# Performance work log

Hardware: AMD Instinct MI355X
Metric: run time of the kernel (lower is better)

## Reference

```python
import jax, jax.numpy as jnp
import numpy as np

# ---------- static mesh topology helpers (numpy, setup-time only) ----------

def _topo_subdivide(nv, faces):
    edge_id = {}
    mids = []
    nf = []
    def mid(a, b):
        k = (a, b) if a < b else (b, a)
        if k not in edge_id:
            edge_id[k] = nv + len(mids)
            mids.append(k)
        return edge_id[k]
    for a, b, c in faces:
        a, b, c = int(a), int(b), int(c)
        ab, bc, ca = mid(a, b), mid(b, c), mid(c, a)
        nf += [[a, ab, ca], [b, bc, ab], [c, ca, bc], [ab, bc, ca]]
    return np.array(nf, dtype=np.int64), np.array(mids, dtype=np.int64)

def _icosphere(level, radius):
    t = (1.0 + 5.0 ** 0.5) / 2.0
    v = np.array([[-1, t, 0], [1, t, 0], [-1, -t, 0], [1, -t, 0],
                  [0, -1, t], [0, 1, t], [0, -1, -t], [0, 1, -t],
                  [t, 0, -1], [t, 0, 1], [-t, 0, -1], [-t, 0, 1]], dtype=np.float64)
    v /= np.linalg.norm(v, axis=1, keepdims=True)
    f = np.array([[0, 11, 5], [0, 5, 1], [0, 1, 7], [0, 7, 10], [0, 10, 11],
                  [1, 5, 9], [5, 11, 4], [11, 10, 2], [10, 7, 6], [7, 1, 8],
                  [3, 9, 4], [3, 4, 2], [3, 2, 6], [3, 6, 8], [3, 8, 9],
                  [4, 9, 5], [2, 4, 11], [6, 2, 10], [8, 6, 7], [9, 8, 1]], dtype=np.int64)
    for _ in range(level):
        f, mids = _topo_subdivide(len(v), f)
        mv = v[mids[:, 0]] + v[mids[:, 1]]
        mv /= np.linalg.norm(mv, axis=1, keepdims=True)
        v = np.concatenate([v, mv], 0)
    return (v * radius).astype(np.float32), f

def _directed_edges(faces):
    e = np.concatenate([faces[:, [0, 1]], faces[:, [1, 2]], faces[:, [2, 0]],
                        faces[:, [1, 0]], faces[:, [2, 1]], faces[:, [0, 2]]], 0)
    return np.unique(e, axis=0).T.astype(np.int64)  # (2, E) directed, deduped

# ---------- jax forward math ----------

def _project(verts, camera_c, camera_f):
    # K @ [I | t], t = (0,0,0.8): rows [f0,0,c0,0.8*c0],[0,f1,c1,0.8*c1],[0,0,1,0.8]
    z = jnp.zeros((), verts.dtype); o = jnp.ones((), verts.dtype)
    tz = jnp.asarray(0.8, verts.dtype)
    P = jnp.stack([
        jnp.stack([camera_f[0], z, camera_c[0], tz * camera_c[0]]),
        jnp.stack([z, camera_f[1], camera_c[1], tz * camera_c[1]]),
        jnp.stack([z, z, o, tz])])
    hom = jnp.concatenate([verts, jnp.ones((verts.shape[0], 1), verts.dtype)], 1)
    pc = hom @ P.T                     # (V, 3)
    return pc[:, :2] / pc[:, 2:3]      # (V, 2) pixel coords [x, y]

def _bilerp(feat, px, py, image_size):
    # feat: (C, dim, dim); px, py: (V,)
    dim = feat.shape[1]
    x = px * dim / image_size
    y = py * dim / image_size
    x1 = jnp.floor(x); x2 = x1 + 1.0
    y1 = jnp.floor(y); y2 = y1 + 1.0
    xi1 = jnp.clip(x1.astype(jnp.int32), 0, dim - 1)
    xi2 = jnp.clip(x2.astype(jnp.int32), 0, dim - 1)
    yi1 = jnp.clip(y1.astype(jnp.int32), 0, dim - 1)
    yi2 = jnp.clip(y2.astype(jnp.int32), 0, dim - 1)
    f11 = feat[:, xi1, yi1].T  # (V, C)
    f12 = feat[:, xi1, yi2].T
    f21 = feat[:, xi2, yi1].T
    f22 = feat[:, xi2, yi2].T
    w11 = ((x2 - x) * (y2 - y))[:, None]
    w12 = ((x2 - x) * (y - y1))[:, None]
    w21 = ((x - x1) * (y2 - y))[:, None]
    w22 = ((x - x1) * (y - y1))[:, None]
    return w11 * f11 + w12 * f12 + w21 * f21 + w22 * f22

def _gconv(x, W0, W1, b, src, dst):
    agg = jax.ops.segment_sum(x[dst], src, num_segments=x.shape[0])
    return x @ W0 + agg @ W1 + b

def _gresnet(x, edges, params):
    Win0, Win1, bin_, W0s, W1s, bs, Wc0, Wc1, bc = params
    src, dst = edges[0], edges[1]
    h = jax.nn.relu(_gconv(x, Win0, Win1, bin_, src, dst))
    def body(h, lw):
        W0, W1, b = lw
        return jax.nn.relu(_gconv(h, W0, W1, b, src, dst)) + h, None
    h, _ = jax.lax.scan(body, h, (W0s, W1s, bs))
    coords = _gconv(h, Wc0, Wc1, bc, src, dst)
    return h, coords

def _forward(f3, f4, f5, verts0, camera_c, camera_f, p1, p2, p3,
             edges1, edges2, edges3, mid0, mid1, image_size):
    def deform(verts, shape_feat, edges, params):
        pix = _project(verts, camera_c, camera_f)
        px, py = pix[:, 0], pix[:, 1]
        perc = jnp.concatenate([_bilerp(f3, px, py, image_size),
                                _bilerp(f4, px, py, image_size),
                                _bilerp(f5, px, py, image_size)], 1)  # (V, 1280)
        feats = jnp.concatenate([perc, shape_feat], 1)
        h, coords = _gresnet(feats, edges, params)
        return coords, h
    def unpool(verts, feat, mid):
        vf = jnp.concatenate([verts, feat], 1)
        new = (vf[mid[:, 0]] + vf[mid[:, 1]]) * 0.5  # edge midpoints
        vf = jnp.concatenate([vf, new], 0)
        return vf[:, :3], vf[:, 3:]
    verts, feat = deform(verts0, verts0, edges1, p1)
    verts, feat = unpool(verts, feat, mid0)
    verts, feat = deform(verts, feat, edges2, p2)
    verts, feat = unpool(verts, feat, mid1)
    verts, _ = deform(verts, feat, edges3, p3)
    return verts  # (40962, 3)

# ---------- harness entry points ----------

def setup_inputs() -> dict:
    key = jax.random.key(0)
    keys = iter(jax.random.split(key, 64))
    v0, f0 = _icosphere(4, 0.2)                      # 2562 verts, 5120 faces
    f1, mid0 = _topo_subdivide(len(v0), f0)          # -> 10242 verts topology
    f2, mid1 = _topo_subdivide(len(v0) + len(mid0), f1)  # -> 40962 verts
    inp = {
        'f3': jax.random.normal(next(keys), (256, 56, 56), jnp.float32),
        'f4': jax.random.normal(next(keys), (512, 28, 28), jnp.float32),
        'f5': jax.random.normal(next(keys), (512, 14, 14), jnp.float32),
        'verts0': jnp.asarray(v0),
        'camera_c': jnp.array([112.0, 112.0], jnp.float32),
        'camera_f': jnp.array([248.0, 248.0], jnp.float32),
    }
    D, L = 128, 12
    def stage(prefix, in_dim):
        def w(shape, scale):
            return jax.random.normal(next(keys), shape, jnp.float32) * scale
        inp[prefix + '_Win0'] = w((in_dim, D), 1.0 / np.sqrt(in_dim))
        inp[prefix + '_Win1'] = w((in_dim, D), 1.0 / np.sqrt(in_dim))
        inp[prefix + '_bin'] = jnp.zeros((D,), jnp.float32)
        inp[prefix + '_W0'] = w((L, D, D), 0.3 / np.sqrt(D))
        inp[prefix + '_W1'] = w((L, D, D), 0.3 / np.sqrt(D))
        inp[prefix + '_b'] = jnp.zeros((L, D), jnp.float32)
        inp[prefix + '_Wc0'] = w((D, 3), 0.01 / np.sqrt(D))
        inp[prefix + '_Wc1'] = w((D, 3), 0.01 / np.sqrt(D))
        inp[prefix + '_bc'] = jnp.zeros((3,), jnp.float32)
    stage('g1', 1283)
    stage('g2', 1408)
    stage('g3', 1408)
    inp['edges1'] = jnp.asarray(_directed_edges(f0))   # (2, 15360)
    inp['edges2'] = jnp.asarray(_directed_edges(f1))   # (2, 61440)
    inp['edges3'] = jnp.asarray(_directed_edges(f2))   # (2, 245760)
    inp['mid0'] = jnp.asarray(mid0)                    # (7680, 2)
    inp['mid1'] = jnp.asarray(mid1)                    # (30720, 2)
    inp['image_size'] = 224
    return inp

def reference(f3, f4, f5, verts0, camera_c, camera_f,
              g1_Win0, g1_Win1, g1_bin, g1_W0, g1_W1, g1_b, g1_Wc0, g1_Wc1, g1_bc,
              g2_Win0, g2_Win1, g2_bin, g2_W0, g2_W1, g2_b, g2_Wc0, g2_Wc1, g2_bc,
              g3_Win0, g3_Win1, g3_bin, g3_W0, g3_W1, g3_b, g3_Wc0, g3_Wc1, g3_bc,
              edges1, edges2, edges3, mid0, mid1, image_size):
    p1 = (g1_Win0, g1_Win1, g1_bin, g1_W0, g1_W1, g1_b, g1_Wc0, g1_Wc1, g1_bc)
    p2 = (g2_Win0, g2_Win1, g2_bin, g2_W0, g2_W1, g2_b, g2_Wc0, g2_Wc1, g2_bc)
    p3 = (g3_Win0, g3_Win1, g3_bin, g3_W0, g3_W1, g3_b, g3_Wc0, g3_Wc1, g3_bc)
    return _forward(f3, f4, f5, verts0, camera_c, camera_f, p1, p2, p3,
                    edges1, edges2, edges3, mid0, mid1, image_size)
```

## Files before the change

kernel.cpp:

```cpp
#include <hip/hip_runtime.h>
#include <hip/hip_bf16.h>
#include <cstddef>
#include <cstdint>

#define DIV_UP(a, b) (((a) + (b) - 1) / (b))

typedef __attribute__((ext_vector_type(8))) short bf16x8v;
typedef __attribute__((ext_vector_type(4))) float f32x4v;

__device__ __forceinline__ unsigned short bf16_rn(float v) {
    unsigned int u = __float_as_uint(v);
    unsigned int r = (u + 0x7FFFu + ((u >> 16) & 1u)) >> 16;
    return (unsigned short)r;
}
__device__ __forceinline__ float bf16_f(unsigned short h) {
    return __uint_as_float(((unsigned int)h) << 16);
}
__device__ __forceinline__ void f2hl(float v, unsigned short& hi, unsigned short& lo) {
    hi = bf16_rn(v);
    float r = v - bf16_f(hi);
    lo = bf16_rn(r);
}

__global__ void transpose_hl(const float* __restrict__ in, unsigned short* __restrict__ ohi,
                             unsigned short* __restrict__ olo, int C, int HW) {
    int idx = blockIdx.x * 256 + threadIdx.x;
    if (idx >= C * HW) return;
    int c = idx % C;
    int p = idx / C;
    float v = in[(size_t)c * HW + p];
    unsigned short hi, lo;
    f2hl(v, hi, lo);
    ohi[(size_t)p * C + c] = hi;
    olo[(size_t)p * C + c] = lo;
}

__global__ void pack_gb_bt(const float* __restrict__ W00, const float* __restrict__ W01,
                           const float* __restrict__ W10, const float* __restrict__ W11,
                           const float* __restrict__ W20, const float* __restrict__ W21,
                           unsigned short* __restrict__ Bhi, unsigned short* __restrict__ Blo,
                           int base, int C) {
    int idx = blockIdx.x * 256 + threadIdx.x;
    if (idx >= 768 * C) return;
    int n = idx / C, k = idx % C;
    int s = n >> 8, j = n & 255;
    const float* W0 = (s == 0) ? W00 : (s == 1) ? W10 : W20;
    const float* W1 = (s == 0) ? W01 : (s == 1) ? W11 : W21;
    float v = (j < 128) ? W0[(size_t)(base + k) * 128 + j]
                        : W1[(size_t)(base + k) * 128 + (j - 128)];
    unsigned short hi, lo;
    f2hl(v, hi, lo);
    Bhi[idx] = hi;
    Blo[idx] = lo;
}

__global__ void pack_lay_bt(const float* __restrict__ W0, const float* __restrict__ W1,
                            unsigned short* __restrict__ Bhi, unsigned short* __restrict__ Blo) {
    int idx = blockIdx.x * 256 + threadIdx.x;
    int l = idx >> 15;
    int r = idx & 32767;
    int n = r >> 8, k = r & 255;
    float v = (k < 128) ? W0[(size_t)l * 16384 + k * 128 + n]
                        : W1[(size_t)l * 16384 + (k - 128) * 128 + n];
    unsigned short hi, lo;
    f2hl(v, hi, lo);
    Bhi[idx] = hi;
    Blo[idx] = lo;
}

__global__ void pack_sh_bt(const float* __restrict__ Win0, const float* __restrict__ Win1,
                           unsigned short* __restrict__ Bhi, unsigned short* __restrict__ Blo) {
    int idx = blockIdx.x * 256 + threadIdx.x;
    if (idx >= 256 * 128) return;
    int n = idx >> 7, k = idx & 127;
    float v = (n < 128) ? Win0[(size_t)(1280 + k) * 128 + n]
                        : Win1[(size_t)(1280 + k) * 128 + (n - 128)];
    unsigned short hi, lo;
    f2hl(v, hi, lo);
    Bhi[idx] = hi;
    Blo[idx] = lo;
}

__global__ void desc_kernel(const float* __restrict__ verts,
                            const float* __restrict__ cam_c, const float* __restrict__ cam_f,
                            const int* __restrict__ imgsz, int V,
                            int* __restrict__ sampi, float* __restrict__ sampw) {
    int v = blockIdx.x * 256 + threadIdx.x;
    if (v >= V) return;
    float X = verts[3 * v + 0], Yy = verts[3 * v + 1], Z = verts[3 * v + 2];
    float cx = cam_c[0], cy = cam_c[1], fx = cam_f[0], fy = cam_f[1];
    const float tz = 0.8f;
    float pz = Z + tz;
    float px = (fx * X + cx * Z + tz * cx) / pz;
    float py = (fy * Yy + cy * Z + tz * cy) / pz;
    float is = (float)imgsz[0];
    const int Ss[3] = {56, 28, 14};
#pragma unroll
    for (int m = 0; m < 3; ++m) {
        int S = Ss[m];
        float dim = (float)S;
        float x = px * dim / is;
        float y = py * dim / is;
        float x1 = floorf(x), y1 = floorf(y);
        float x2 = x1 + 1.0f, y2 = y1 + 1.0f;
        float smax = (float)(S - 1);
        int xi1 = (int)fminf(fmaxf(x1, 0.0f), smax);
        int xi2 = (int)fminf(fmaxf(x2, 0.0f), smax);
        int yi1 = (int)fminf(fmaxf(y1, 0.0f), smax);
        int yi2 = (int)fminf(fmaxf(y2, 0.0f), smax);
        int b = v * 12 + m * 4;
        sampi[b + 0] = xi1 * S + yi1;
        sampi[b + 1] = xi1 * S + yi2;
        sampi[b + 2] = xi2 * S + yi1;
        sampi[b + 3] = xi2 * S + yi2;
        sampw[b + 0] = (x2 - x) * (y2 - y);
        sampw[b + 1] = (x2 - x) * (y - y1);
        sampw[b + 2] = (x - x1) * (y2 - y);
        sampw[b + 3] = (x - x1) * (y - y1);
    }
}

__global__ void rowptr_kernel(const int* __restrict__ src, int E, int V, int* __restrict__ rowptr) {
    int v = blockIdx.x * 256 + threadIdx.x;
    if (v > V) return;
    int lo = 0, hi = E;
    while (lo < hi) {
        int mid = (lo + hi) >> 1;
        if (src[mid] < v) lo = mid + 1; else hi = mid;
    }
    rowptr[v] = lo;
}

struct MArgs {
    const unsigned short *Ahi, *Alo; int lda;
    const unsigned short *Bhi, *Blo; int K;
    float* Y;
    int sstr;
    int V;
};

template <int EPI>
__global__ __launch_bounds__(256) void mgemm(MArgs g) {
    __shared__ unsigned short As_hi[64][40], As_lo[64][40];
    __shared__ unsigned short Bs_hi[128][40], Bs_lo[128][40];
    int tid = threadIdx.x;
    int row0 = blockIdx.y * 64;
    int col0 = blockIdx.x * 128;
    int l = tid & 63, wid = tid >> 6;
    int wr = wid & 1, wc = wid >> 1;
    int lw = l & 15, gg = l >> 4;
    f32x4v acc[2][4];
#pragma unroll
    for (int i = 0; i < 2; ++i)
#pragma unroll
        for (int j = 0; j < 4; ++j) acc[i][j] = (f32x4v){0.f, 0.f, 0.f, 0.f};

    int arow = tid >> 2, akoff = (tid & 3) * 8;
    for (int k0 = 0; k0 < g.K; k0 += 32) {
        __syncthreads();
        {
            int grow = row0 + arow;
            uint4 zh = make_uint4(0, 0, 0, 0), zl = make_uint4(0, 0, 0, 0);
            if (grow < g.V) {
                zh = *(const uint4*)(g.Ahi + (size_t)grow * g.lda + k0 + akoff);
                zl = *(const uint4*)(g.Alo + (size_t)grow * g.lda + k0 + akoff);
            }
            *(uint4*)&As_hi[arow][akoff] = zh;
            *(uint4*)&As_lo[arow][akoff] = zl;
        }
#pragma unroll
        for (int it = 0; it < 2; ++it) {
            int q = tid + it * 256;
            int n = q >> 2, koff = (q & 3) * 8;
            *(uint4*)&Bs_hi[n][koff] = *(const uint4*)(g.Bhi + (size_t)(col0 + n) * g.K + k0 + koff);
            *(uint4*)&Bs_lo[n][koff] = *(const uint4*)(g.Blo + (size_t)(col0 + n) * g.K + k0 + koff);
        }
        __syncthreads();
        bf16x8v ah[2], al[2], bh[4], bl[4];
#pragma unroll
        for (int mt = 0; mt < 2; ++mt) {
            int r = wr * 32 + mt * 16 + lw;
            ah[mt] = *(const bf16x8v*)&As_hi[r][gg * 8];
            al[mt] = *(const bf16x8v*)&As_lo[r][gg * 8];
        }
#pragma unroll
        for (int nt = 0; nt < 4; ++nt) {
            int c = wc * 64 + nt * 16 + lw;
            bh[nt] = *(const bf16x8v*)&Bs_hi[c][gg * 8];
            bl[nt] = *(const bf16x8v*)&Bs_lo[c][gg * 8];
        }
#pragma unroll
        for (int mt = 0; mt < 2; ++mt)
#pragma unroll
            for (int nt = 0; nt < 4; ++nt) {
                acc[mt][nt] = __builtin_amdgcn_mfma_f32_16x16x32_bf16(ah[mt], bh[nt], acc[mt][nt], 0, 0, 0);
                acc[mt][nt] = __builtin_amdgcn_mfma_f32_16x16x32_bf16(ah[mt], bl[nt], acc[mt][nt], 0, 0, 0);
                acc[mt][nt] = __builtin_amdgcn_mfma_f32_16x16x32_bf16(al[mt], bh[nt], acc[mt][nt], 0, 0, 0);
            }
    }
#pragma unroll
    for (int mt = 0; mt < 2; ++mt)
#pragma unroll
        for (int nt = 0; nt < 4; ++nt) {
            int colg = wc * 64 + nt * 16 + lw;
#pragma unroll
            for (int r = 0; r < 4; ++r) {
                int rowg = row0 + wr * 32 + mt * 16 + gg * 4 + r;
                if (rowg >= g.V) continue;
                float v = acc[mt][nt][r];
                if (EPI == 0) {
                    g.Y[(size_t)rowg * 256 + col0 + colg] += v;
                } else {
                    int cg = col0 + colg;
                    g.Y[(size_t)(cg >> 8) * g.sstr + (size_t)rowg * 256 + (cg & 255)] = v;
                }
            }
        }
}

__global__ void gather_kernel(const float* __restrict__ G, int sstr,
                              const int* __restrict__ sampi, const float* __restrict__ sampw,
                              float* __restrict__ Yb, int V, int stage,
                              const float* __restrict__ Win0, const float* __restrict__ Win1,
                              const float* __restrict__ shape) {
    int v = blockIdx.x;
    if (v >= V) return;
    int j = threadIdx.x;
    const float* Gs = G + (size_t)stage * sstr;
    int b = v * 12;
    float acc = 0.0f;
#pragma unroll
    for (int s = 0; s < 4; ++s)
        acc += sampw[b + s] * Gs[(size_t)sampi[b + s] * 256 + j];
#pragma unroll
    for (int s = 0; s < 4; ++s)
        acc += sampw[b + 4 + s] * Gs[(size_t)(3136 + sampi[b + 4 + s]) * 256 + j];
#pragma unroll
    for (int s = 0; s < 4; ++s)
        acc += sampw[b + 8 + s] * Gs[(size_t)(3920 + sampi[b + 8 + s]) * 256 + j];
    if (stage == 0) {
#pragma unroll
        for (int k = 0; k < 3; ++k) {
            float w = shape[v * 3 + k];
            float wv = (j < 128) ? Win0[(size_t)(1280 + k) * 128 + j]
                                 : Win1[(size_t)(1280 + k) * 128 + (j - 128)];
            acc += w * wv;
        }
    }
    Yb[(size_t)v * 256 + j] = acc;
}

__global__ __launch_bounds__(256) void combine_in(
    const float* __restrict__ Y, const float* __restrict__ bias,
    const int* __restrict__ rowptr, const int* __restrict__ dst,
    float* __restrict__ hout, int V) {
    int v = blockIdx.x * 2 + (threadIdx.x >> 7);
    int d = threadIdx.x & 127;
    if (v >= V) return;
    float val = Y[(size_t)v * 256 + d] + bias[d];
    int e0 = rowptr[v], e1 = rowptr[v + 1];
    for (int e = e0; e < e1; ++e) val += Y[(size_t)dst[e] * 256 + 128 + d];
    val = fmaxf(val, 0.0f);
    hout[(size_t)v * 128 + d] = val;
}

struct LArgs {
    const float* h;
    const unsigned short *Bhi, *Blo;
    const int *rowptr, *dst;
    const float* bias;
    float* hnext;
    int V;
};

__global__ __launch_bounds__(256) void lay_kernel(LArgs g) {
    __shared__ unsigned short As_hi[64][40], As_lo[64][40];
    __shared__ unsigned short Bs_hi[128][40], Bs_lo[128][40];
    int tid = threadIdx.x;

    int nwg = gridDim.x;
    int orig = blockIdx.x;
    int qq = nwg >> 3, rr = nwg & 7;
    int xcd = orig & 7, idx = orig >> 3;
    int bid = (xcd < rr ? xcd * (qq + 1) : rr * (qq + 1) + (xcd - rr) * qq) + idx;
    int row0 = bid * 64;

    int l = tid & 63, wid = tid >> 6;
    int wr = wid & 1, wc = wid >> 1;
    int lw = l & 15, gg = l >> 4;
    int arow = tid >> 2;
    int aq = tid & 3;
    int grow = row0 + arow;

    f32x4v acc[2][4];
#pragma unroll
    for (int i = 0; i < 2; ++i)
#pragma unroll
        for (int j = 0; j < 4; ++j) acc[i][j] = (f32x4v){0.f, 0.f, 0.f, 0.f};

    float vals[32];

    auto mfma_step = [&](int ks, int kglob0) {
        uint4 b0h, b1h, b0l, b1l;
        {
            int n0 = tid >> 2, koff = (tid & 3) * 8;
            b0h = *(const uint4*)(g.Bhi + (size_t)n0 * 256 + kglob0 + koff);
            b0l = *(const uint4*)(g.Blo + (size_t)n0 * 256 + kglob0 + koff);
            int n1 = n0 + 64;
            b1h = *(const uint4*)(g.Bhi + (size_t)n1 * 256 + kglob0 + koff);
            b1l = *(const uint4*)(g.Blo + (size_t)n1 * 256 + kglob0 + koff);
        }
        if (aq == ks) {
            unsigned short hh[8], ll[8];
#pragma unroll
            for (int c = 0; c < 4; ++c) {
#pragma unroll
                for (int i = 0; i < 8; ++i) f2hl(vals[c * 8 + i], hh[i], ll[i]);
                *(uint4*)&As_hi[arow][c * 8] = *(uint4*)hh;
                *(uint4*)&As_lo[arow][c * 8] = *(uint4*)ll;
            }
        }
        {
            int n0 = tid >> 2, koff = (tid & 3) * 8;
            *(uint4*)&Bs_hi[n0][koff] = b0h;
            *(uint4*)&Bs_lo[n0][koff] = b0l;
            *(uint4*)&Bs_hi[n0 + 64][koff] = b1h;
            *(uint4*)&Bs_lo[n0 + 64][koff] = b1l;
        }
        __syncthreads();
        bf16x8v ah[2], al[2], bh[4], bl[4];
#pragma unroll
        for (int mt = 0; mt < 2; ++mt) {
            int r = wr * 32 + mt * 16 + lw;
            ah[mt] = *(const bf16x8v*)&As_hi[r][gg * 8];
            al[mt] = *(const bf16x8v*)&As_lo[r][gg * 8];
        }
#pragma unroll
        for (int nt = 0; nt < 4; ++nt) {
            int c = wc * 64 + nt * 16 + lw;
            bh[nt] = *(const bf16x8v*)&Bs_hi[c][gg * 8];
            bl[nt] = *(const bf16x8v*)&Bs_lo[c][gg * 8];
        }
#pragma unroll
        for (int mt = 0; mt < 2; ++mt)
#pragma unroll
            for (int nt = 0; nt < 4; ++nt) {
                acc[mt][nt] = __builtin_amdgcn_mfma_f32_16x16x32_bf16(ah[mt], bh[nt], acc[mt][nt], 0, 0, 0);
                acc[mt][nt] = __builtin_amdgcn_mfma_f32_16x16x32_bf16(ah[mt], bl[nt], acc[mt][nt], 0, 0, 0);
                acc[mt][nt] = __builtin_amdgcn_mfma_f32_16x16x32_bf16(al[mt], bh[nt], acc[mt][nt], 0, 0, 0);
            }
        __syncthreads();
    };

    if (grow < g.V) {
        const float* hp = g.h + (size_t)grow * 128 + aq * 32;
#pragma unroll
        for (int c = 0; c < 8; ++c) {
            float4 f = *(const float4*)(hp + c * 4);
            vals[c * 4 + 0] = f.x;
            vals[c * 4 + 1] = f.y;
            vals[c * 4 + 2] = f.z;
            vals[c * 4 + 3] = f.w;
        }
    } else {
#pragma unroll
        for (int i = 0; i < 32; ++i) vals[i] = 0.0f;
    }
    for (int ks = 0; ks < 4; ++ks) mfma_step(ks, ks * 32);

#pragma unroll
    for (int i = 0; i < 32; ++i) vals[i] = 0.0f;
    if (grow < g.V) {
        int e0 = g.rowptr[grow], e1 = g.rowptr[grow + 1];
        for (int e = e0; e < e1; ++e) {
            const float* hp = g.h + (size_t)g.dst[e] * 128 + aq * 32;
#pragma unroll
            for (int c = 0; c < 8; ++c) {
                float4 f = *(const float4*)(hp + c * 4);
                vals[c * 4 + 0] += f.x;
                vals[c * 4 + 1] += f.y;
                vals[c * 4 + 2] += f.z;
                vals[c * 4 + 3] += f.w;
            }
        }
    }
    for (int ks = 0; ks < 4; ++ks) mfma_step(ks, 128 + ks * 32);

#pragma unroll
    for (int mt = 0; mt < 2; ++mt)
#pragma unroll
        for (int nt = 0; nt < 4; ++nt) {
            int colg = wc * 64 + nt * 16 + lw;
            float bv = g.bias[colg];
#pragma unroll
            for (int r = 0; r < 4; ++r) {
                int rowg = row0 + wr * 32 + mt * 16 + gg * 4 + r;
                if (rowg >= g.V) continue;
                float v = acc[mt][nt][r] + bv;
                v = fmaxf(v, 0.0f);
                v += g.h[(size_t)rowg * 128 + colg];
                g.hnext[(size_t)rowg * 128 + colg] = v;
            }
        }
}

__global__ void coordgemm_kernel(const float* __restrict__ h,
                                 const float* __restrict__ Wc0, const float* __restrict__ Wc1,
                                 int V, float* __restrict__ Yc) {
    int idx = blockIdx.x * 256 + threadIdx.x;
    if (idx >= V * 6) return;
    int v = idx / 6, j = idx % 6;
    const float* W = (j < 3) ? Wc0 : Wc1;
    int jj = (j < 3) ? j : j - 3;
    const float* hp = h + (size_t)v * 128;
    float acc = 0.0f;
#pragma unroll
    for (int k = 0; k < 32; ++k) {
        float4 f = *(const float4*)(hp + k * 4);
        acc += f.x * W[(k * 4 + 0) * 3 + jj];
        acc += f.y * W[(k * 4 + 1) * 3 + jj];
        acc += f.z * W[(k * 4 + 2) * 3 + jj];
        acc += f.w * W[(k * 4 + 3) * 3 + jj];
    }
    Yc[idx] = acc;
}

__global__ void coordcombine_kernel(const float* __restrict__ Yc, const float* __restrict__ bc,
                                    const int* __restrict__ rowptr, const int* __restrict__ dst,
                                    int V, float* __restrict__ out) {
    int idx = blockIdx.x * 256 + threadIdx.x;
    if (idx >= V * 3) return;
    int v = idx / 3, j = idx % 3;
    float val = Yc[(size_t)v * 6 + j] + bc[j];
    int e0 = rowptr[v], e1 = rowptr[v + 1];
    for (int e = e0; e < e1; ++e) val += Yc[(size_t)dst[e] * 6 + 3 + j];
    out[(size_t)v * 3 + j] = val;
}

__global__ void unpool_kernel(float* __restrict__ verts, const float* __restrict__ h,
                              const int* __restrict__ mid, int V, int Nm,
                              unsigned short* __restrict__ fphi, unsigned short* __restrict__ fplo) {
    int r = blockIdx.x;
    int t = threadIdx.x;
    if (r < V) {
        float v = h[(size_t)r * 128 + t];
        unsigned short hi, lo;
        f2hl(v, hi, lo);
        fphi[(size_t)r * 128 + t] = hi;
        fplo[(size_t)r * 128 + t] = lo;
    } else {
        int i = r - V;
        int a = mid[2 * i], b = mid[2 * i + 1];
        float v = 0.5f * (h[(size_t)a * 128 + t] + h[(size_t)b * 128 + t]);
        unsigned short hi, lo;
        f2hl(v, hi, lo);
        fphi[(size_t)r * 128 + t] = hi;
        fplo[(size_t)r * 128 + t] = lo;
        if (t < 3)
            verts[(size_t)r * 3 + t] = 0.5f * (verts[(size_t)a * 3 + t] + verts[(size_t)b * 3 + t]);
    }
}

extern "C" void kernel_launch(void* const* d_in, const int* in_sizes, int n_in,
                              void* d_out, int out_size, void* d_ws, size_t ws_size,
                              hipStream_t stream) {
    const float* f3 = (const float*)d_in[0];
    const float* f4 = (const float*)d_in[1];
    const float* f5 = (const float*)d_in[2];
    const float* verts0 = (const float*)d_in[3];
    const float* cam_c = (const float*)d_in[4];
    const float* cam_f = (const float*)d_in[5];
    const int* imgsz = (const int*)d_in[38];

    int V0 = in_sizes[3] / 3;
    int E[3] = {in_sizes[33] / 2, in_sizes[34] / 2, in_sizes[35] / 2};
    int Nm0 = in_sizes[36] / 2, Nm1 = in_sizes[37] / 2;
    int V1 = V0 + Nm0, V2 = V1 + Nm1;
    int Vs[3] = {V0, V1, V2};
    const int NPIXT = 3136 + 784 + 196;
    const int GS = NPIXT * 256;

    char* wsp = (char*)d_ws;
    auto alloc = [&](size_t bytes) -> void* {
        void* p = (void*)wsp;
        wsp += (bytes + 255) & ~(size_t)255;
        return p;
    };
    unsigned short* ft0h = (unsigned short*)alloc((size_t)3136 * 256 * 2);
    unsigned short* ft0l = (unsigned short*)alloc((size_t)3136 * 256 * 2);
    unsigned short* ft1h = (unsigned short*)alloc((size_t)784 * 512 * 2);
    unsigned short* ft1l = (unsigned short*)alloc((size_t)784 * 512 * 2);
    unsigned short* ft2h = (unsigned short*)alloc((size_t)196 * 512 * 2);
    unsigned short* ft2l = (unsigned short*)alloc((size_t)196 * 512 * 2);
    unsigned short* Bg0h = (unsigned short*)alloc((size_t)768 * 256 * 2);
    unsigned short* Bg0l = (unsigned short*)alloc((size_t)768 * 256 * 2);
    unsigned short* Bg1h = (unsigned short*)alloc((size_t)768 * 512 * 2);
    unsigned short* Bg1l = (unsigned short*)alloc((size_t)768 * 512 * 2);
    unsigned short* Bg2h = (unsigned short*)alloc((size_t)768 * 512 * 2);
    unsigned short* Bg2l = (unsigned short*)alloc((size_t)768 * 512 * 2);
    float* Gbuf = (float*)alloc((size_t)3 * GS * 4);
    unsigned short* BtLhi = (unsigned short*)alloc((size_t)12 * 128 * 256 * 2);
    unsigned short* BtLlo = (unsigned short*)alloc((size_t)12 * 128 * 256 * 2);
    unsigned short* BtShi = (unsigned short*)alloc((size_t)256 * 128 * 2);
    unsigned short* BtSlo = (unsigned short*)alloc((size_t)256 * 128 * 2);
    float* Ybuf = (float*)alloc((size_t)V2 * 256 * 4);
    float* hA = (float*)alloc((size_t)V2 * 128 * 4);
    float* hB = (float*)alloc((size_t)V2 * 128 * 4);
    unsigned short* FPhi = (unsigned short*)alloc((size_t)V2 * 128 * 2);
    unsigned short* FPlo = (unsigned short*)alloc((size_t)V2 * 128 * 2);
    float* vertsbuf = (float*)alloc((size_t)V2 * 3 * 4);
    float* Yc = (float*)alloc((size_t)V2 * 6 * 4);
    int* sampi = (int*)alloc((size_t)V2 * 12 * 4);
    float* sampw = (float*)alloc((size_t)V2 * 12 * 4);
    int* rowptr = (int*)alloc(((size_t)V2 + 1) * 4);

    transpose_hl<<<DIV_UP(256 * 56 * 56, 256), 256, 0, stream>>>(f3, ft0h, ft0l, 256, 56 * 56);
    transpose_hl<<<DIV_UP(512 * 28 * 28, 256), 256, 0, stream>>>(f4, ft1h, ft1l, 512, 28 * 28);
    transpose_hl<<<DIV_UP(512 * 14 * 14, 256), 256, 0, stream>>>(f5, ft2h, ft2l, 512, 14 * 14);

    const float* W0s_[3] = {(const float*)d_in[6], (const float*)d_in[15], (const float*)d_in[24]};
    const float* W1s_[3] = {(const float*)d_in[7], (const float*)d_in[16], (const float*)d_in[25]};

    pack_gb_bt<<<DIV_UP(768 * 256, 256), 256, 0, stream>>>(W0s_[0], W1s_[0], W0s_[1], W1s_[1],
                                                           W0s_[2], W1s_[2], Bg0h, Bg0l, 0, 256);
    pack_gb_bt<<<DIV_UP(768 * 512, 256), 256, 0, stream>>>(W0s_[0], W1s_[0], W0s_[1], W1s_[1],
                                                           W0s_[2], W1s_[2], Bg1h, Bg1l, 256, 512);
    pack_gb_bt<<<DIV_UP(768 * 512, 256), 256, 0, stream>>>(W0s_[0], W1s_[0], W0s_[1], W1s_[1],
                                                           W0s_[2], W1s_[2], Bg2h, Bg2l, 768, 512);
    {
        MArgs m = {};
        m.sstr = GS;
        m.Ahi = ft0h; m.Alo = ft0l; m.lda = 256;
        m.Bhi = Bg0h; m.Blo = Bg0l; m.K = 256;
        m.Y = Gbuf; m.V = 3136;
        dim3 g0(6, DIV_UP(3136, 64));
        mgemm<2><<<g0, 256, 0, stream>>>(m);
        m.Ahi = ft1h; m.Alo = ft1l; m.lda = 512;
        m.Bhi = Bg1h; m.Blo = Bg1l; m.K = 512;
        m.Y = Gbuf + (size_t)3136 * 256; m.V = 784;
        dim3 g1(6, DIV_UP(784, 64));
        mgemm<2><<<g1, 256, 0, stream>>>(m);
        m.Ahi = ft2h; m.Alo = ft2l; m.lda = 512;
        m.Bhi = Bg2h; m.Blo = Bg2l; m.K = 512;
        m.Y = Gbuf + (size_t)3920 * 256; m.V = 196;
        dim3 g2(6, DIV_UP(196, 64));
        mgemm<2><<<g2, 256, 0, stream>>>(m);
    }

    for (int si = 0; si < 3; ++si) {
        const float* Win0 = (const float*)d_in[6 + si * 9 + 0];
        const float* Win1 = (const float*)d_in[6 + si * 9 + 1];
        const float* bin = (const float*)d_in[6 + si * 9 + 2];
        const float* W0L = (const float*)d_in[6 + si * 9 + 3];
        const float* W1L = (const float*)d_in[6 + si * 9 + 4];
        const float* bs = (const float*)d_in[6 + si * 9 + 5];
        const float* Wc0 = (const float*)d_in[6 + si * 9 + 6];
        const float* Wc1 = (const float*)d_in[6 + si * 9 + 7];
        const float* bc = (const float*)d_in[6 + si * 9 + 8];
        const int* edges = (const int*)d_in[33 + si];
        int Ecur = E[si];
        const int* esrc = edges;
        const int* edst = edges + Ecur;
        int V = Vs[si];
        const float* vertsin = (si == 0) ? verts0 : vertsbuf;

        pack_lay_bt<<<12 * 128, 256, 0, stream>>>(W0L, W1L, BtLhi, BtLlo);
        if (si > 0) pack_sh_bt<<<128, 256, 0, stream>>>(Win0, Win1, BtShi, BtSlo);
        desc_kernel<<<DIV_UP(V, 256), 256, 0, stream>>>(vertsin, cam_c, cam_f, imgsz, V,
                                                        sampi, sampw);
        rowptr_kernel<<<DIV_UP(V + 1, 256), 256, 0, stream>>>(esrc, Ecur, V, rowptr);

        gather_kernel<<<V, 256, 0, stream>>>(Gbuf, GS, sampi, sampw, Ybuf, V, si, Win0, Win1,
                                             (si == 0) ? verts0 : nullptr);
        if (si > 0) {
            MArgs m = {};
            m.Ahi = FPhi; m.Alo = FPlo; m.lda = 128;
            m.Bhi = BtShi; m.Blo = BtSlo; m.K = 128;
            m.Y = Ybuf; m.V = V;
            dim3 grid(2, DIV_UP(V, 64));
            mgemm<0><<<grid, 256, 0, stream>>>(m);
        }
        combine_in<<<DIV_UP(V, 2), 256, 0, stream>>>(Ybuf, bin, rowptr, edst, hA, V);

        float* hcur = hA;
        float* hnext = hB;
        for (int ll = 0; ll < 12; ++ll) {
            LArgs a = {};
            a.h = hcur;
            a.Bhi = BtLhi + (size_t)ll * 32768;
            a.Blo = BtLlo + (size_t)ll * 32768;
            a.rowptr = rowptr; a.dst = edst;
            a.bias = bs + (size_t)ll * 128;
            a.hnext = hnext;
            a.V = V;
            lay_kernel<<<DIV_UP(V, 64), 256, 0, stream>>>(a);
            float* t = hcur; hcur = hnext; hnext = t;
        }

        coordgemm_kernel<<<DIV_UP(V * 6, 256), 256, 0, stream>>>(hcur, Wc0, Wc1, V, Yc);
        float* ctarget = (si == 2) ? (float*)d_out : vertsbuf;
        coordcombine_kernel<<<DIV_UP(V * 3, 256), 256, 0, stream>>>(Yc, bc, rowptr, edst, V,
                                                                    ctarget);
        if (si < 2) {
            const int* mid = (const int*)d_in[36 + si];
            int Nm = (si == 0) ? Nm0 : Nm1;
            unpool_kernel<<<V + Nm, 128, 0, stream>>>(vertsbuf, hcur, mid, V, Nm, FPhi, FPlo);
        }
    }
}
```

Measured before the change: 1.511 ms.

## Replace CSR rowptr with fixed-width adjacency table and batch weight packing

Merges all weight-packing launches into one pack_all kernel, with separate per-stage buffers so packing no longer runs inside the stage loop. Replaces the rowptr/dst CSR walk with a padded 8-slot neighbour table built in the descriptor kernel, and unrolls neighbour loops to 6 entries. It also reorders the shape GEMM before the gather so the gather accumulates into the GEMM output, and applies XCD block swizzling to gather and combine. The aim is fewer launches and fewer dependent index loads, at the cost of assuming vertex degree is at most 6.

```diff
diff --git a/kernel.cpp b/kernel.cpp
--- a/kernel.cpp
+++ b/kernel.cpp
@@ -20,6 +20,11 @@
     hi = bf16_rn(v);
     float r = v - bf16_f(hi);
     lo = bf16_rn(r);
+}
+__device__ __forceinline__ int xcd_swz(int orig, int nwg) {
+    int q = nwg >> 3, r = nwg & 7;
+    int xcd = orig & 7, idx = orig >> 3;
+    return (xcd < r ? xcd * (q + 1) : r * (q + 1) + (xcd - r) * q) + idx;
 }
 
 __global__ void transpose_hl(const float* __restrict__ in, unsigned short* __restrict__ ohi,
@@ -35,56 +40,66 @@
     olo[(size_t)p * C + c] = lo;
 }
 
-__global__ void pack_gb_bt(const float* __restrict__ W00, const float* __restrict__ W01,
-                           const float* __restrict__ W10, const float* __restrict__ W11,
-                           const float* __restrict__ W20, const float* __restrict__ W21,
-                           unsigned short* __restrict__ Bhi, unsigned short* __restrict__ Blo,
-                           int base, int C) {
+struct PackArgs {
+    const float* Win0[3]; const float* Win1[3];
+    const float* W0L[3];  const float* W1L[3];
+    unsigned short *BtLhi[3], *BtLlo[3];
+    unsigned short *BtShi[2], *BtSlo[2];
+    unsigned short *Bgh[3], *Bgl[3];
+};
+
+__global__ void pack_all(PackArgs p) {
+    const int LAY1 = 12 * 128 * 256;
+    const int LAYT = 3 * LAY1;
+    const int SH1 = 256 * 128;
+    const int SHT = 2 * SH1;
+    const int GB0 = 768 * 256, GB1 = 768 * 512;
     int idx = blockIdx.x * 256 + threadIdx.x;
-    if (idx >= 768 * C) return;
-    int n = idx / C, k = idx % C;
-    int s = n >> 8, j = n & 255;
-    const float* W0 = (s == 0) ? W00 : (s == 1) ? W10 : W20;
-    const float* W1 = (s == 0) ? W01 : (s == 1) ? W11 : W21;
-    float v = (j < 128) ? W0[(size_t)(base + k) * 128 + j]
-                        : W1[(size_t)(base + k) * 128 + (j - 128)];
+    float v;
+    unsigned short* dh;
+    unsigned short* dl;
+    size_t o;
+    if (idx < LAYT) {
+        int st = idx / LAY1, r = idx % LAY1;
+        int l = r >> 15, rr = r & 32767;
+        int n = rr >> 8, k = rr & 255;
+        v = (k < 128) ? p.W0L[st][(size_t)l * 16384 + k * 128 + n]
+                      : p.W1L[st][(size_t)l * 16384 + (k - 128) * 128 + n];
+        dh = p.BtLhi[st]; dl = p.BtLlo[st]; o = r;
+    } else if (idx < LAYT + SHT) {
+        int q = idx - LAYT;
+        int st = q / SH1, rr = q % SH1;
+        int n = rr >> 7, k = rr & 127;
+        const float* w0 = p.Win0[st + 1];
+        const float* w1 = p.Win1[st + 1];
+        v = (n < 128) ? w0[(size_t)(1280 + k) * 128 + n]
+                      : w1[(size_t)(1280 + k) * 128 + (n - 128)];
+        dh = p.BtShi[st]; dl = p.BtSlo[st]; o = rr;
+    } else {
+        int q = idx - LAYT - SHT;
+        int m, C, base;
+        if (q < GB0) { m = 0; C = 256; base = 0; }
+        else if (q < GB0 + GB1) { m = 1; C = 512; base = 256; q -= GB0; }
+        else if (q < GB0 + 2 * GB1) { m = 2; C = 512; base = 768; q -= GB0 + GB1; }
+        else return;
+        int n = q / C, k = q % C;
+        int s = n >> 8, j = n & 255;
+        v = (j < 128) ? p.Win0[s][(size_t)(base + k) * 128 + j]
+                      : p.Win1[s][(size_t)(base + k) * 128 + (j - 128)];
+        dh = p.Bgh[m]; dl = p.Bgl[m]; o = q;
+    }
     unsigned short hi, lo;
     f2hl(v, hi, lo);
-    Bhi[idx] = hi;
-    Blo[idx] = lo;
-}
-
-__global__ void pack_lay_bt(const float* __restrict__ W0, const float* __restrict__ W1,
-                            unsigned short* __restrict__ Bhi, unsigned short* __restrict__ Blo) {
-    int idx = blockIdx.x * 256 + threadIdx.x;
-    int l = idx >> 15;
-    int r = idx & 32767;
-    int n = r >> 8, k = r & 255;
-    float v = (k < 128) ? W0[(size_t)l * 16384 + k * 128 + n]
-                        : W1[(size_t)l * 16384 + (k - 128) * 128 + n];
-    unsigned short hi, lo;
-    f2hl(v, hi, lo);
-    Bhi[idx] = hi;
-    Blo[idx] = lo;
-}
-
-__global__ void pack_sh_bt(const float* __restrict__ Win0, const float* __restrict__ Win1,
-                           unsigned short* __restrict__ Bhi, unsigned short* __restrict__ Blo) {
-    int idx = blockIdx.x * 256 + threadIdx.x;
-    if (idx >= 256 * 128) return;
-    int n = idx >> 7, k = idx & 127;
-    float v = (n < 128) ? Win0[(size_t)(1280 + k) * 128 + n]
-                        : Win1[(size_t)(1280 + k) * 128 + (n - 128)];
-    unsigned short hi, lo;
-    f2hl(v, hi, lo);
-    Bhi[idx] = hi;
-    Blo[idx] = lo;
-}
-
-__global__ void desc_kernel(const float* __restrict__ verts,
-                            const float* __restrict__ cam_c, const float* __restrict__ cam_f,
-                            const int* __restrict__ imgsz, int V,
-                            int* __restrict__ sampi, float* __restrict__ sampw) {
+    dh[o] = hi;
+    dl[o] = lo;
+}
+
+__global__ void desc_adj_kernel(const float* __restrict__ verts,
+                                const float* __restrict__ cam_c, const float* __restrict__ cam_f,
+                                const int* __restrict__ imgsz, int V,
+                                const int* __restrict__ src, const int* __restrict__ dst, int E,
+                                int* __restrict__ sampi, float* __restrict__ sampw,
+                                int* __restrict__ adj8) {
     int v = blockIdx.x * 256 + threadIdx.x;
     if (v >= V) return;
     float X = verts[3 * v + 0], Yy = verts[3 * v + 1], Z = verts[3 * v + 2];
@@ -118,17 +133,18 @@
         sampw[b + 2] = (x - x1) * (y2 - y);
         sampw[b + 3] = (x - x1) * (y - y1);
     }
-}
-
-__global__ void rowptr_kernel(const int* __restrict__ src, int E, int V, int* __restrict__ rowptr) {
-    int v = blockIdx.x * 256 + threadIdx.x;
-    if (v > V) return;
     int lo = 0, hi = E;
-    while (lo < hi) {
-        int mid = (lo + hi) >> 1;
-        if (src[mid] < v) lo = mid + 1; else hi = mid;
-    }
-    rowptr[v] = lo;
+    while (lo < hi) { int m = (lo + hi) >> 1; if (src[m] < v) lo = m + 1; else hi = m; }
+    int e0 = lo;
+    hi = E;
+    while (lo < hi) { int m = (lo + hi) >> 1; if (src[m] < v + 1) lo = m + 1; else hi = m; }
+    int e1 = lo;
+    int* ap = adj8 + (size_t)v * 8;
+#pragma unroll
+    for (int i = 0; i < 8; ++i) {
+        int e = e0 + i;
+        ap[i] = (e < e1) ? dst[e] : -1;
+    }
 }
 
 struct MArgs {
@@ -208,8 +224,8 @@
                 int rowg = row0 + wr * 32 + mt * 16 + gg * 4 + r;
                 if (rowg >= g.V) continue;
                 float v = acc[mt][nt][r];
-                if (EPI == 0) {
-                    g.Y[(size_t)rowg * 256 + col0 + colg] += v;
+                if (EPI == 3) {
+                    g.Y[(size_t)rowg * 256 + col0 + colg] = v;
                 } else {
                     int cg = col0 + colg;
                     g.Y[(size_t)(cg >> 8) * g.sstr + (size_t)rowg * 256 + (cg & 255)] = v;
@@ -223,12 +239,12 @@
                               float* __restrict__ Yb, int V, int stage,
                               const float* __restrict__ Win0, const float* __restrict__ Win1,
                               const float* __restrict__ shape) {
-    int v = blockIdx.x;
+    int v = xcd_swz(blockIdx.x, gridDim.x);
     if (v >= V) return;
     int j = threadIdx.x;
     const float* Gs = G + (size_t)stage * sstr;
     int b = v * 12;
-    float acc = 0.0f;
+    float acc = (stage == 0) ? 0.0f : Yb[(size_t)v * 256 + j];
 #pragma unroll
     for (int s = 0; s < 4; ++s)
         acc += sampw[b + s] * Gs[(size_t)sampi[b + s] * 256 + j];
@@ -252,14 +268,20 @@
 
 __global__ __launch_bounds__(256) void combine_in(
     const float* __restrict__ Y, const float* __restrict__ bias,
-    const int* __restrict__ rowptr, const int* __restrict__ dst,
+    const int* __restrict__ adj8,
     float* __restrict__ hout, int V) {
-    int v = blockIdx.x * 2 + (threadIdx.x >> 7);
+    int bid = xcd_swz(blockIdx.x, gridDim.x);
+    int v = bid * 2 + (threadIdx.x >> 7);
     int d = threadIdx.x & 127;
     if (v >= V) return;
     float val = Y[(size_t)v * 256 + d] + bias[d];
-    int e0 = rowptr[v], e1 = rowptr[v + 1];
-    for (int e = e0; e < e1; ++e) val += Y[(size_t)dst[e] * 256 + 128 + d];
+    const int* ap = adj8 + (size_t)v * 8;
+    int n[6];
+#pragma unroll
+    for (int i = 0; i < 6; ++i) n[i] = ap[i];
+#pragma unroll
+    for (int i = 0; i < 6; ++i)
+        if (n[i] >= 0) val += Y[(size_t)n[i] * 256 + 128 + d];
     val = fmaxf(val, 0.0f);
     hout[(size_t)v * 128 + d] = val;
 }
@@ -267,7 +289,7 @@
 struct LArgs {
     const float* h;
     const unsigned short *Bhi, *Blo;
-    const int *rowptr, *dst;
+    const int* adj8;
     const float* bias;
     float* hnext;
     int V;
@@ -277,13 +299,7 @@
     __shared__ unsigned short As_hi[64][40], As_lo[64][40];
     __shared__ unsigned short Bs_hi[128][40], Bs_lo[128][40];
     int tid = threadIdx.x;
-
-    int nwg = gridDim.x;
-    int orig = blockIdx.x;
-    int qq = nwg >> 3, rr = nwg & 7;
-    int xcd = orig & 7, idx = orig >> 3;
-    int bid = (xcd < rr ? xcd * (qq + 1) : rr * (qq + 1) + (xcd - rr) * qq) + idx;
-    int row0 = bid * 64;
+    int row0 = xcd_swz(blockIdx.x, gridDim.x) * 64;
 
     int l = tid & 63, wid = tid >> 6;
     int wr = wid & 1, wc = wid >> 1;
@@ -371,16 +387,22 @@
 #pragma unroll
     for (int i = 0; i < 32; ++i) vals[i] = 0.0f;
     if (grow < g.V) {
-        int e0 = g.rowptr[grow], e1 = g.rowptr[grow + 1];
-        for (int e = e0; e < e1; ++e) {
-            const float* hp = g.h + (size_t)g.dst[e] * 128 + aq * 32;
-#pragma unroll
-            for (int c = 0; c < 8; ++c) {
-                float4 f = *(const float4*)(hp + c * 4);
-                vals[c * 4 + 0] += f.x;
-                vals[c * 4 + 1] += f.y;
-                vals[c * 4 + 2] += f.z;
-                vals[c * 4 + 3] += f.w;
+        const int* ap = g.adj8 + (size_t)grow * 8;
+        int n[6];
+#pragma unroll
+        for (int i = 0; i < 6; ++i) n[i] = ap[i];
+#pragma unroll
+        for (int i = 0; i < 6; ++i) {
+            if (n[i] >= 0) {
+                const float* hp = g.h + (size_t)n[i] * 128 + aq * 32;
+#pragma unroll
+                for (int c = 0; c < 8; ++c) {
+                    float4 f = *(const float4*)(hp + c * 4);
+                    vals[c * 4 + 0] += f.x;
+                    vals[c * 4 + 1] += f.y;
+                    vals[c * 4 + 2] += f.z;
+                    vals[c * 4 + 3] += f.w;
+                }
             }
         }
     }
@@ -426,14 +448,19 @@
 }
 
 __global__ void coordcombine_kernel(const float* __restrict__ Yc, const float* __restrict__ bc,
-                                    const int* __restrict__ rowptr, const int* __restrict__ dst,
+                                    const int* __restrict__ adj8,
                                     int V, float* __restrict__ out) {
     int idx = blockIdx.x * 256 + threadIdx.x;
     if (idx >= V * 3) return;
     int v = idx / 3, j = idx % 3;
     float val = Yc[(size_t)v * 6 + j] + bc[j];
-    int e0 = rowptr[v], e1 = rowptr[v + 1];
-    for (int e = e0; e < e1; ++e) val += Yc[(size_t)dst[e] * 6 + 3 + j];
+    const int* ap = adj8 + (size_t)v * 8;
+    int n[6];
+#pragma unroll
+    for (int i = 0; i < 6; ++i) n[i] = ap[i];
+#pragma unroll
+    for (int i = 0; i < 6; ++i)
+        if (n[i] >= 0) val += Yc[(size_t)n[i] * 6 + 3 + j];
     out[(size_t)v * 3 + j] = val;
 }
 
@@ -499,10 +526,18 @@
     unsigned short* Bg2h = (unsigned short*)alloc((size_t)768 * 512 * 2);
     unsigned short* Bg2l = (unsigned short*)alloc((size_t)768 * 512 * 2);
     float* Gbuf = (float*)alloc((size_t)3 * GS * 4);
-    unsigned short* BtLhi = (unsigned short*)alloc((size_t)12 * 128 * 256 * 2);
-    unsigned short* BtLlo = (unsigned short*)alloc((size_t)12 * 128 * 256 * 2);
-    unsigned short* BtShi = (unsigned short*)alloc((size_t)256 * 128 * 2);
-    unsigned short* BtSlo = (unsigned short*)alloc((size_t)256 * 128 * 2);
+    unsigned short* BtLhi[3];
+    unsigned short* BtLlo[3];
+    for (int s = 0; s < 3; ++s) {
+        BtLhi[s] = (unsigned short*)alloc((size_t)12 * 128 * 256 * 2);
+        BtLlo[s] = (unsigned short*)alloc((size_t)12 * 128 * 256 * 2);
+    }
+    unsigned short* BtShi[2];
+    unsigned short* BtSlo[2];
+    for (int s = 0; s < 2; ++s) {
+        BtShi[s] = (unsigned short*)alloc((size_t)256 * 128 * 2);
+        BtSlo[s] = (unsigned short*)alloc((size_t)256 * 128 * 2);
+    }
     float* Ybuf = (float*)alloc((size_t)V2 * 256 * 4);
     float* hA = (float*)alloc((size_t)V2 * 128 * 4);
     float* hB = (float*)alloc((size_t)V2 * 128 * 4);
@@ -512,21 +547,30 @@
     float* Yc = (float*)alloc((size_t)V2 * 6 * 4);
     int* sampi = (int*)alloc((size_t)V2 * 12 * 4);
     float* sampw = (float*)alloc((size_t)V2 * 12 * 4);
-    int* rowptr = (int*)alloc(((size_t)V2 + 1) * 4);
+    int* adj8 = (int*)alloc((size_t)V2 * 8 * 4);
 
     transpose_hl<<<DIV_UP(256 * 56 * 56, 256), 256, 0, stream>>>(f3, ft0h, ft0l, 256, 56 * 56);
     transpose_hl<<<DIV_UP(512 * 28 * 28, 256), 256, 0, stream>>>(f4, ft1h, ft1l, 512, 28 * 28);
     transpose_hl<<<DIV_UP(512 * 14 * 14, 256), 256, 0, stream>>>(f5, ft2h, ft2l, 512, 14 * 14);
 
-    const float* W0s_[3] = {(const float*)d_in[6], (const float*)d_in[15], (const float*)d_in[24]};
-    const float* W1s_[3] = {(const float*)d_in[7], (const float*)d_in[16], (const float*)d_in[25]};
-
-    pack_gb_bt<<<DIV_UP(768 * 256, 256), 256, 0, stream>>>(W0s_[0], W1s_[0], W0s_[1], W1s_[1],
-                                                           W0s_[2], W1s_[2], Bg0h, Bg0l, 0, 256);
-    pack_gb_bt<<<DIV_UP(768 * 512, 256), 256, 0, stream>>>(W0s_[0], W1s_[0], W0s_[1], W1s_[1],
-                                                           W0s_[2], W1s_[2], Bg1h, Bg1l, 256, 512);
-    pack_gb_bt<<<DIV_UP(768 * 512, 256), 256, 0, stream>>>(W0s_[0], W1s_[0], W0s_[1], W1s_[1],
-                                                           W0s_[2], W1s_[2], Bg2h, Bg2l, 768, 512);
+    {
+        PackArgs p;
+        for (int s = 0; s < 3; ++s) {
+            p.Win0[s] = (const float*)d_in[6 + s * 9 + 0];
+            p.Win1[s] = (const float*)d_in[6 + s * 9 + 1];
+            p.W0L[s] = (const float*)d_in[6 + s * 9 + 3];
+            p.W1L[s] = (const float*)d_in[6 + s * 9 + 4];
+            p.BtLhi[s] = BtLhi[s]; p.BtLlo[s] = BtLlo[s];
+        }
+        p.BtShi[0] = BtShi[0]; p.BtSlo[0] = BtSlo[0];
+        p.BtShi[1] = BtShi[1]; p.BtSlo[1] = BtSlo[1];
+        p.Bgh[0] = Bg0h; p.Bgl[0] = Bg0l;
+        p.Bgh[1] = Bg1h; p.Bgl[1] = Bg1l;
+        p.Bgh[2] = Bg2h; p.Bgl[2] = Bg2l;
+        int total = 3 * 12 * 128 * 256 + 2 * 256 * 128 + 768 * 256 + 2 * 768 * 512;
+        pack_all<<<DIV_UP(total, 256), 256, 0, stream>>>(p);
+    }
+
     {
         MArgs m = {};
         m.sstr = GS;
@@ -551,8 +595,6 @@
         const float* Win0 = (const float*)d_in[6 + si * 9 + 0];
         const float* Win1 = (const float*)d_in[6 + si * 9 + 1];
         const float* bin = (const float*)d_in[6 + si * 9 + 2];
-        const float* W0L = (const float*)d_in[6 + si * 9 + 3];
-        const float* W1L = (const float*)d_in[6 + si * 9 + 4];
         const float* bs = (const float*)d_in[6 + si * 9 + 5];
         const float* Wc0 = (const float*)d_in[6 + si * 9 + 6];
         const float* Wc1 = (const float*)d_in[6 + si * 9 + 7];
@@ -564,32 +606,28 @@
         int V = Vs[si];
         const float* vertsin = (si == 0) ? verts0 : vertsbuf;
 
-        pack_lay_bt<<<12 * 128, 256, 0, stream>>>(W0L, W1L, BtLhi, BtLlo);
-        if (si > 0) pack_sh_bt<<<128, 256, 0, stream>>>(Win0, Win1, BtShi, BtSlo);
-        desc_kernel<<<DIV_UP(V, 256), 256, 0, stream>>>(vertsin, cam_c, cam_f, imgsz, V,
-                                                        sampi, sampw);
-        rowptr_kernel<<<DIV_UP(V + 1, 256), 256, 0, stream>>>(esrc, Ecur, V, rowptr);
-
-        gather_kernel<<<V, 256, 0, stream>>>(Gbuf, GS, sampi, sampw, Ybuf, V, si, Win0, Win1,
-                                             (si == 0) ? verts0 : nullptr);
+        desc_adj_kernel<<<DIV_UP(V, 256), 256, 0, stream>>>(vertsin, cam_c, cam_f, imgsz, V,
+                                                            esrc, edst, Ecur, sampi, sampw, adj8);
         if (si > 0) {
             MArgs m = {};
             m.Ahi = FPhi; m.Alo = FPlo; m.lda = 128;
-            m.Bhi = BtShi; m.Blo = BtSlo; m.K = 128;
+            m.Bhi = BtShi[si - 1]; m.Blo = BtSlo[si - 1]; m.K = 128;
             m.Y = Ybuf; m.V = V;
             dim3 grid(2, DIV_UP(V, 64));
-            mgemm<0><<<grid, 256, 0, stream>>>(m);
-        }
-        combine_in<<<DIV_UP(V, 2), 256, 0, stream>>>(Ybuf, bin, rowptr, edst, hA, V);
+            mgemm<3><<<grid, 256, 0, stream>>>(m);
+        }
+        gather_kernel<<<V, 256, 0, stream>>>(Gbuf, GS, sampi, sampw, Ybuf, V, si, Win0, Win1,
+                                             (si == 0) ? verts0 : nullptr);
+        combine_in<<<DIV_UP(V, 2), 256, 0, stream>>>(Ybuf, bin, adj8, hA, V);
 
         float* hcur = hA;
         float* hnext = hB;
         for (int ll = 0; ll < 12; ++ll) {
             LArgs a = {};
             a.h = hcur;
-            a.Bhi = BtLhi + (size_t)ll * 32768;
-            a.Blo = BtLlo + (size_t)ll * 32768;
-            a.rowptr = rowptr; a.dst = edst;
+            a.Bhi = BtLhi[si] + (size_t)ll * 32768;
+            a.Blo = BtLlo[si] + (size_t)ll * 32768;
+            a.adj8 = adj8;
             a.bias = bs + (size_t)ll * 128;
             a.hnext = hnext;
             a.V = V;
@@ -599,8 +637,7 @@
 
         coordgemm_kernel<<<DIV_UP(V * 6, 256), 256, 0, stream>>>(hcur, Wc0, Wc1, V, Yc);
         float* ctarget = (si == 2) ? (float*)d_out : vertsbuf;
-        coordcombine_kernel<<<DIV_UP(V * 3, 256), 256, 0, stream>>>(Yc, bc, rowptr, edst, V,
-                                                                    ctarget);
+        coordcombine_kernel<<<DIV_UP(V * 3, 256), 256, 0, stream>>>(Yc, bc, adj8, V, ctarget);
         if (si < 2) {
             const int* mid = (const int*)d_in[36 + si];
             int Nm = (si == 0) ? Nm0 : Nm1;
```

Measured after the change: 1.418 ms. 1.07x faster.
